# Kernel optimization log

Hardware: AMD Instinct MI355X
Metric: run time of the kernel (lower is better)

Reference implementation:

```python
import jax, jax.numpy as jnp
import numpy as np

N_HEAD = 16
LN_EPS = 1e-5


def _layernorm(x, g, b):
    mu = jnp.mean(x, axis=-1, keepdims=True)
    var = jnp.mean(jnp.square(x - mu), axis=-1, keepdims=True)
    return (x - mu) * jax.lax.rsqrt(var + LN_EPS) * g + b


def setup_inputs() -> dict:
    key = jax.random.key(0)
    ks = jax.random.split(key, 12)
    B, S, D = 2, 2048, 1024
    F = 4 * D
    std = 0.02
    return {
        "x": jax.random.normal(ks[0], (B, S, D), jnp.float32),
        "w_attn": jax.random.normal(ks[1], (D, 3 * D), jnp.float32) * std,
        "b_attn": jnp.zeros((3 * D,), jnp.float32),
        "w_o": jax.random.normal(ks[2], (D, D), jnp.float32) * std,
        "b_o": jnp.zeros((D,), jnp.float32),
        "ln1_g": jnp.ones((D,), jnp.float32),
        "ln1_b": jnp.zeros((D,), jnp.float32),
        "w_fc": jax.random.normal(ks[3], (D, F), jnp.float32) * std,
        "b_fc": jnp.zeros((F,), jnp.float32),
        "w_pr": jax.random.normal(ks[4], (F, D), jnp.float32) * std,
        "b_pr": jnp.zeros((D,), jnp.float32),
        "ln2_g": jnp.ones((D,), jnp.float32),
        "ln2_b": jnp.zeros((D,), jnp.float32),
    }


def reference(x, w_attn, b_attn, w_o, b_o, ln1_g, ln1_b,
              w_fc, b_fc, w_pr, b_pr, ln2_g, ln2_b):
    B, S, D = x.shape
    H = N_HEAD
    hd = D // H

    # --- attention ---
    qkv = x @ w_attn + b_attn                      # [B,S,3D]
    q, k, v = jnp.split(qkv, 3, axis=-1)
    q = q.reshape(B, S, H, hd).transpose(0, 2, 1, 3)  # [B,H,S,hd]
    k = k.reshape(B, S, H, hd).transpose(0, 2, 1, 3)
    v = v.reshape(B, S, H, hd).transpose(0, 2, 1, 3)

    # scores in fp32, scaled by sqrt(head_dim) (scale=True)
    w = jnp.einsum('bhqd,bhkd->bhqk', q.astype(jnp.float32),
                   k.astype(jnp.float32)) / jnp.sqrt(jnp.float32(hd))
    bias = jnp.tril(jnp.ones((S, S), jnp.float32))     # causal mask slice of registered buffer
    w = w * bias + (-10000.0) * (1.0 - bias)
    a = jax.nn.softmax(w, axis=-1).astype(v.dtype)
    o = jnp.einsum('bhqk,bhkd->bhqd', a, v)            # [B,H,S,hd]
    o = o.transpose(0, 2, 1, 3).reshape(B, S, D)
    a_out = o @ w_o + b_o

    # --- post-LN residual + MLP (gelu, d_ff = 4D) ---
    n = _layernorm(x + a_out, ln1_g, ln1_b)
    m = jax.nn.gelu(n @ w_fc + b_fc, approximate=False) @ w_pr + b_pr
    h = _layernorm(n + m, ln2_g, ln2_b)
    return h
```

## Files before the change

kernel.cpp:

```cpp
#include <hip/hip_runtime.h>
#include <stdint.h>
#include <math.h>


typedef __attribute__((ext_vector_type(4))) float f32x4;
typedef __attribute__((ext_vector_type(8))) short s16x8;

__device__ __forceinline__ float bf2f(short s){
  unsigned u = ((unsigned)(unsigned short)s) << 16;
  return __builtin_bit_cast(float, u);
}
__device__ __forceinline__ short f2bf(float f){
  unsigned u = __builtin_bit_cast(unsigned, f);
  unsigned r = (u + 0x7fffu + ((u >> 16) & 1u)) >> 16;
  return (short)(unsigned short)r;
}

__device__ __forceinline__ void gload_lds16(const void* gp, void* lp){
  __builtin_amdgcn_global_load_lds(
      (__attribute__((address_space(1))) void*)const_cast<void*>(gp),
      (__attribute__((address_space(3))) void*)lp,
      16, 0, 0);
}

__global__ void cvt_f32_bf16(const float* __restrict__ in, short* __restrict__ out, int n){
  int i = (blockIdx.x * blockDim.x + threadIdx.x) * 4;
  if (i < n){
    float4 v = *(const float4*)(in + i);
    short4 o;
    o.x = f2bf(v.x); o.y = f2bf(v.y); o.z = f2bf(v.z); o.w = f2bf(v.w);
    *(short4*)(out + i) = o;
  }
}

__global__ __launch_bounds__(256) void wtrans(const float* __restrict__ in,
                                              short* __restrict__ out, int R, int C){
  __shared__ float tile[32][33];
  int c0 = blockIdx.x * 32, r0 = blockIdx.y * 32;
  int tx = threadIdx.x, ty = threadIdx.y;
  #pragma unroll
  for (int j = 0; j < 4; ++j)
    tile[ty + j*8][tx] = in[(size_t)(r0 + ty + j*8) * C + c0 + tx];
  __syncthreads();
  #pragma unroll
  for (int j = 0; j < 4; ++j)
    out[(size_t)(c0 + ty + j*8) * R + r0 + tx] = f2bf(tile[tx][ty + j*8]);
}

__global__ __launch_bounds__(256) void vtrans(const short* __restrict__ qkv,
                                              short* __restrict__ vt){
  __shared__ short tile[32][33];
  int bh = blockIdx.z; int b = bh >> 4, h = bh & 15;
  int s0 = blockIdx.x * 32, d0 = blockIdx.y * 32;
  int tx = threadIdx.x, ty = threadIdx.y;
  #pragma unroll
  for (int j = 0; j < 4; ++j)
    tile[ty + j*8][tx] = qkv[(size_t)(b*2048 + s0 + ty + j*8) * 3072 + 2048 + h*64 + d0 + tx];
  __syncthreads();
  #pragma unroll
  for (int j = 0; j < 4; ++j)
    vt[(size_t)(bh*64 + d0 + ty + j*8) * 2048 + s0 + tx] = tile[tx][ty + j*8];
}

#define GBM 128
#define GBN 128
#define GBK 64

__global__ __launch_bounds__(256, 4) void gemm_bf16(
    const short* __restrict__ A, const short* __restrict__ BT,
    const float* __restrict__ bias,
    void* __restrict__ out, void* __restrict__ out2,
    void* __restrict__ out3, void* __restrict__ out4,
    int M, int N, int K, int EPI, int KS)
{
  __shared__ short sA[GBM * GBK];
  __shared__ short sB[GBN * GBK];
  const int t = threadIdx.x;
  const int lane = t & 63;
  const int w = t >> 6;
  const int wr = w >> 1, wc = w & 1;
  const int lrow = lane & 15;
  const int lk = lane >> 4;

  const int gx = gridDim.x;
  const int nwg = gx * gridDim.y;
  const int P = blockIdx.y * gx + blockIdx.x;
  const int wg = (P & 7) * (nwg >> 3) + (P >> 3);
  const int m0 = (wg / gx) * GBM, n0 = (wg % gx) * GBN;

  const int Kspl = K / KS;
  const int kbeg = blockIdx.z * Kspl;

  f32x4 acc[4][4] = {};

  for (int kk = kbeg; kk < kbeg + Kspl; kk += GBK){
    __syncthreads();
    #pragma unroll
    for (int r = 0; r < 4; ++r){
      int o = r * 4096 + t * 16;
      int row = o >> 7;
      int phys = (o >> 4) & 7;
      int lsl = phys ^ (row & 7);
      gload_lds16(A + (size_t)(m0 + row) * K + kk + lsl * 8, (char*)sA + o);
    }
    #pragma unroll
    for (int r = 0; r < 4; ++r){
      int o = r * 4096 + t * 16;
      int row = o >> 7;
      int phys = (o >> 4) & 7;
      int lsl = phys ^ (row & 7);
      gload_lds16(BT + (size_t)(n0 + row) * K + kk + lsl * 8, (char*)sB + o);
    }
    __syncthreads();

    #pragma unroll
    for (int kc = 0; kc < 2; ++kc){
      s16x8 af[4], bf[4];
      #pragma unroll
      for (int rt = 0; rt < 4; ++rt){
        int row = wr*64 + rt*16 + lrow;
        int slot = (kc*4 + lk) ^ (row & 7);
        af[rt] = *(const s16x8*)&sA[row*64 + slot*8];
      }
      #pragma unroll
      for (int ct = 0; ct < 4; ++ct){
        int row = wc*64 + ct*16 + lrow;
        int slot = (kc*4 + lk) ^ (row & 7);
        bf[ct] = *(const s16x8*)&sB[row*64 + slot*8];
      }
      #pragma unroll
      for (int rt = 0; rt < 4; ++rt)
        #pragma unroll
        for (int ct = 0; ct < 4; ++ct)
          acc[rt][ct] = __builtin_amdgcn_mfma_f32_16x16x32_bf16(af[rt], bf[ct], acc[rt][ct], 0, 0, 0);
    }
  }

  void* pz = (blockIdx.z == 0) ? out : (blockIdx.z == 1) ? out2
           : (blockIdx.z == 2) ? out3 : out4;
  #pragma unroll
  for (int rt = 0; rt < 4; ++rt){
    #pragma unroll
    for (int ct = 0; ct < 4; ++ct){
      #pragma unroll
      for (int r = 0; r < 4; ++r){
        int row = m0 + wr*64 + rt*16 + lk*4 + r;
        int col = n0 + wc*64 + ct*16 + lrow;
        size_t idx = (size_t)row * N + col;
        if (EPI == 4){
          ((short*)pz)[idx] = f2bf(acc[rt][ct][r]);
        } else {
          float v = acc[rt][ct][r] + bias[col];
          if (EPI == 0){
            ((short*)out)[idx] = f2bf(v);
          } else {
            float g = 0.5f * v * (1.0f + erff(v * 0.70710678118654752f));
            ((short*)out)[idx] = f2bf(g);
          }
        }
      }
    }
  }
}

__global__ __launch_bounds__(256, 2) void attn_kernel(
    const short* __restrict__ qkv, const short* __restrict__ vt,
    short* __restrict__ ob)
{
  const int P = blockIdx.x;
  const int xcd = P & 7;
  const int idx = P >> 3;
  const int pairi = idx & 15;
  const int bh = xcd + ((idx >> 4) << 3);
  const int b = bh >> 4, h = bh & 15;
  const int t  = threadIdx.x;
  const int lane = t & 63;
  const int w = t >> 6;
  const int lrow = lane & 15, lk = lane >> 4;

  __shared__ short sK[2][64*64];
  __shared__ short sV[2][64*64];
  __shared__ short sP[4][16][68];

  const size_t kgbase = (size_t)(b*2048)*3072 + 1024 + h*64;
  const size_t vgbase = (size_t)((b*16 + h)*64)*2048;

  s16x8 bones;
  #pragma unroll
  for (int i = 0; i < 8; ++i) bones[i] = (short)0x3F80;

  auto stage = [&](int buf, int k0){
    #pragma unroll
    for (int r2 = 0; r2 < 2; ++r2){
      int o = r2*4096 + t*16;
      int row = o >> 7;
      int lsl = ((o >> 4) & 7) ^ (row & 7);
      gload_lds16(qkv + kgbase + (size_t)(k0 + row)*3072 + lsl*8, (char*)sK[buf] + o);
      gload_lds16(vt  + vgbase + (size_t)row*2048 + k0   + lsl*8, (char*)sV[buf] + o);
    }
  };

  for (int pass = 0; pass < 2; ++pass){
    const int qt = pass ? 31 - pairi : pairi;
    const int q0 = qt * 64;
    const int qbase = q0 + w * 16;

    s16x8 aq[2];
    #pragma unroll
    for (int kc = 0; kc < 2; ++kc)
      aq[kc] = *(const s16x8*)(qkv + (size_t)(b*2048 + qbase + lrow)*3072 + h*64 + kc*32 + lk*8);

    f32x4 oacc[4] = {};
    f32x4 sumacc = {};

    const int nt = qt + 1;
    __syncthreads();
    stage(0, 0);
    __syncthreads();
    int cur = 0;

    for (int ktile = 0; ktile < nt; ++ktile){
      const int k0 = ktile * 64;
      if (ktile + 1 < nt) stage(cur ^ 1, k0 + 64);

      f32x4 sacc[4] = {};
      __builtin_amdgcn_s_setprio(1);
      #pragma unroll
      for (int kc = 0; kc < 2; ++kc){
        #pragma unroll
        for (int ct = 0; ct < 4; ++ct){
          int row = ct*16 + lrow;
          int slot = (kc*4 + lk) ^ (row & 7);
          s16x8 bk = *(const s16x8*)&sK[cur][row*64 + slot*8];
          sacc[ct] = __builtin_amdgcn_mfma_f32_16x16x32_bf16(aq[kc], bk, sacc[ct], 0, 0, 0);
        }
      }
      __builtin_amdgcn_s_setprio(0);

      const bool need_mask = (k0 + 63 > qbase);
      #pragma unroll
      for (int ct = 0; ct < 4; ++ct){
        #pragma unroll
        for (int r = 0; r < 4; ++r){
          float v = sacc[ct][r] * 0.125f;
          if (need_mask){
            int qi = qbase + lk*4 + r;
            int ki = k0 + ct*16 + lrow;
            if (ki > qi) v = -10000.0f;
          }
          sP[w][lk*4 + r][ct*16 + lrow] = f2bf(__expf(v));
        }
      }

      s16x8 pa[2];
      #pragma unroll
      for (int kc = 0; kc < 2; ++kc)
        pa[kc] = *(const s16x8*)&sP[w][lrow][kc*32 + lk*8];
      __builtin_amdgcn_s_setprio(1);
      #pragma unroll
      for (int dt = 0; dt < 4; ++dt){
        #pragma unroll
        for (int kc = 0; kc < 2; ++kc){
          int row = dt*16 + lrow;
          int slot = (kc*4 + lk) ^ (row & 7);
          s16x8 bv = *(const s16x8*)&sV[cur][row*64 + slot*8];
          oacc[dt] = __builtin_amdgcn_mfma_f32_16x16x32_bf16(pa[kc], bv, oacc[dt], 0, 0, 0);
        }
      }
      #pragma unroll
      for (int kc = 0; kc < 2; ++kc)
        sumacc = __builtin_amdgcn_mfma_f32_16x16x32_bf16(pa[kc], bones, sumacc, 0, 0, 0);
      __builtin_amdgcn_s_setprio(0);

      __syncthreads();
      cur ^= 1;
    }

    #pragma unroll
    for (int r = 0; r < 4; ++r){
      float inv = 1.0f / sumacc[r];
      int row = b*2048 + qbase + lk*4 + r;
      #pragma unroll
      for (int dt = 0; dt < 4; ++dt){
        int col = h*64 + dt*16 + lrow;
        ob[(size_t)row * 1024 + col] = f2bf(oacc[dt][r] * inv);
      }
    }
  }
}

__global__ __launch_bounds__(256) void ln_fused(
    const short* __restrict__ p0, const short* __restrict__ p1,
    const short* __restrict__ p2, const short* __restrict__ p3,
    const float* __restrict__ bias,
    const short* __restrict__ resid_bf, const float* __restrict__ resid_f,
    const float* __restrict__ g, const float* __restrict__ b,
    void* __restrict__ out, int bf16_out)
{
  const int row = blockIdx.x;
  const int t = threadIdx.x;
  const size_t base = (size_t)row*1024 + t*4;
  short4 a0 = *(const short4*)(p0 + base);
  short4 a1 = *(const short4*)(p1 + base);
  short4 a2 = *(const short4*)(p2 + base);
  short4 a3 = *(const short4*)(p3 + base);
  float4 bi = *(const float4*)(bias + t*4);
  float r0, r1, r2, r3;
  if (resid_bf){
    short4 rr = *(const short4*)(resid_bf + base);
    r0 = bf2f(rr.x); r1 = bf2f(rr.y); r2 = bf2f(rr.z); r3 = bf2f(rr.w);
  } else {
    float4 rr = *(const float4*)(resid_f + base);
    r0 = rr.x; r1 = rr.y; r2 = rr.z; r3 = rr.w;
  }
  float v0 = bf2f(a0.x) + bf2f(a1.x) + bf2f(a2.x) + bf2f(a3.x) + bi.x + r0;
  float v1 = bf2f(a0.y) + bf2f(a1.y) + bf2f(a2.y) + bf2f(a3.y) + bi.y + r1;
  float v2 = bf2f(a0.z) + bf2f(a1.z) + bf2f(a2.z) + bf2f(a3.z) + bi.z + r2;
  float v3 = bf2f(a0.w) + bf2f(a1.w) + bf2f(a2.w) + bf2f(a3.w) + bi.w + r3;
  float s = v0 + v1 + v2 + v3;
  float q = v0*v0 + v1*v1 + v2*v2 + v3*v3;
  #pragma unroll
  for (int off = 1; off < 64; off <<= 1){
    s += __shfl_xor(s, off, 64);
    q += __shfl_xor(q, off, 64);
  }
  __shared__ float ss[4], sq[4];
  if ((t & 63) == 0){ ss[t >> 6] = s; sq[t >> 6] = q; }
  __syncthreads();
  s = ss[0] + ss[1] + ss[2] + ss[3];
  q = sq[0] + sq[1] + sq[2] + sq[3];
  float mu = s * (1.0f/1024.0f);
  float var = q * (1.0f/1024.0f) - mu*mu;
  float rs = rsqrtf(var + 1e-5f);
  float4 gg = *(const float4*)(g + t*4);
  float4 bb = *(const float4*)(b + t*4);
  float o0 = (v0 - mu)*rs*gg.x + bb.x;
  float o1 = (v1 - mu)*rs*gg.y + bb.y;
  float o2 = (v2 - mu)*rs*gg.z + bb.z;
  float o3 = (v3 - mu)*rs*gg.w + bb.w;
  if (bf16_out){
    short4 o; o.x = f2bf(o0); o.y = f2bf(o1); o.z = f2bf(o2); o.w = f2bf(o3);
    *(short4*)((short*)out + base) = o;
  } else {
    float4 o = {o0, o1, o2, o3};
    *(float4*)((float*)out + base) = o;
  }
}

extern "C" void kernel_launch(void* const* d_in, const int* in_sizes, int n_in,
                              void* d_out, int out_size, void* d_ws, size_t ws_size,
                              hipStream_t stream) {
  const float* x      = (const float*)d_in[0];
  const float* w_attn = (const float*)d_in[1];
  const float* b_attn = (const float*)d_in[2];
  const float* w_o    = (const float*)d_in[3];
  const float* b_o    = (const float*)d_in[4];
  const float* ln1_g  = (const float*)d_in[5];
  const float* ln1_b  = (const float*)d_in[6];
  const float* w_fc   = (const float*)d_in[7];
  const float* b_fc   = (const float*)d_in[8];
  const float* w_pr   = (const float*)d_in[9];
  const float* b_pr   = (const float*)d_in[10];
  const float* ln2_g  = (const float*)d_in[11];
  const float* ln2_b  = (const float*)d_in[12];

  char* ws = (char*)d_ws;
  const size_t MB = 1048576;
  short* waT  = (short*)(ws + 0);
  short* wfT  = (short*)(ws + 6*MB);
  short* wpT  = (short*)(ws + 14*MB);
  short* woT  = (short*)(ws + 22*MB);
  short* xb   = (short*)(ws + 24*MB);
  short* vt   = (short*)(ws + 24*MB);
  short* pp2  = (short*)(ws + 24*MB);
  short* qkvb = (short*)(ws + 32*MB);
  short* fb   = (short*)(ws + 32*MB);
  short* ob   = (short*)(ws + 56*MB);
  short* pp0  = (short*)(ws + 64*MB);
  short* pp1  = (short*)(ws + 72*MB);
  short* nb   = (short*)(ws + 80*MB);
  short* pp3  = (short*)(ws + 88*MB);

  const int M = 4096;

  cvt_f32_bf16<<<dim3(M*1024/1024), dim3(256), 0, stream>>>(x, xb, M*1024);
  wtrans<<<dim3(3072/32, 1024/32), dim3(32,8), 0, stream>>>(w_attn, waT, 1024, 3072);
  wtrans<<<dim3(1024/32, 1024/32), dim3(32,8), 0, stream>>>(w_o,   woT, 1024, 1024);
  wtrans<<<dim3(4096/32, 1024/32), dim3(32,8), 0, stream>>>(w_fc,  wfT, 1024, 4096);
  wtrans<<<dim3(1024/32, 4096/32), dim3(32,8), 0, stream>>>(w_pr,  wpT, 4096, 1024);
  gemm_bf16<<<dim3(3072/GBN, M/GBM), dim3(256), 0, stream>>>(
      xb, waT, b_attn, qkvb, nullptr, nullptr, nullptr, M, 3072, 1024, 0, 1);
  vtrans<<<dim3(2048/32, 64/32, 32), dim3(32,8), 0, stream>>>(qkvb, vt);
  attn_kernel<<<dim3(512), dim3(256), 0, stream>>>(qkvb, vt, ob);
  gemm_bf16<<<dim3(1024/GBN, M/GBM, 4), dim3(256), 0, stream>>>(
      ob, woT, nullptr, pp0, pp1, pp2, pp3, M, 1024, 1024, 4, 4);
  ln_fused<<<dim3(M), dim3(256), 0, stream>>>(pp0, pp1, pp2, pp3, b_o,
                                              nullptr, x, ln1_g, ln1_b, nb, 1);
  gemm_bf16<<<dim3(4096/GBN, M/GBM), dim3(256), 0, stream>>>(
      nb, wfT, b_fc, fb, nullptr, nullptr, nullptr, M, 4096, 1024, 2, 1);
  gemm_bf16<<<dim3(1024/GBN, M/GBM, 4), dim3(256), 0, stream>>>(
      fb, wpT, nullptr, pp0, pp1, pp2, pp3, M, 1024, 4096, 4, 4);
  ln_fused<<<dim3(M), dim3(256), 0, stream>>>(pp0, pp1, pp2, pp3, b_pr,
                                              nb, nullptr, ln2_g, ln2_b, d_out, 0);
}
```

Before: 254.8 us.

## Stage GEMM epilogue through LDS, fold softmax scale into QKV, widen attention blocks

The GEMM epilogue now writes results into swizzled shared memory and then issues 16-byte coalesced global stores instead of scattered 2-byte stores. The QKV GEMM pre-multiplies Q by log2(e)/sqrt(hd), so attention can use exp2f without a per-score scale. The attention kernel now runs 512 threads: two warp sets process the paired short and long query tiles together over shared K/V stages. It also uses explicit vmcnt waits and raw barriers, so the next tile's loads overlap compute. These changes add shared-memory traffic and an extra barrier in the GEMM, and make the attention synchronisation more delicate.

```diff
diff --git a/kernel.cpp b/kernel.cpp
--- a/kernel.cpp
+++ b/kernel.cpp
@@ -22,6 +22,8 @@
       (__attribute__((address_space(3))) void*)lp,
       16, 0, 0);
 }
+
+#define QSCALE 0.18033688f
 
 __global__ void cvt_f32_bf16(const float* __restrict__ in, short* __restrict__ out, int n){
   int i = (blockIdx.x * blockDim.x + threadIdx.x) * 4;
@@ -73,8 +75,9 @@
     void* __restrict__ out3, void* __restrict__ out4,
     int M, int N, int K, int EPI, int KS)
 {
-  __shared__ short sA[GBM * GBK];
-  __shared__ short sB[GBN * GBK];
+  __shared__ __attribute__((aligned(16))) short smem[GBM*GBK*2];
+  short* sA = smem;
+  short* sB = smem + GBM*GBK;
   const int t = threadIdx.x;
   const int lane = t & 63;
   const int w = t >> 6;
@@ -136,42 +139,55 @@
     }
   }
 
-  void* pz = (blockIdx.z == 0) ? out : (blockIdx.z == 1) ? out2
-           : (blockIdx.z == 2) ? out3 : out4;
+  __syncthreads();
   #pragma unroll
   for (int rt = 0; rt < 4; ++rt){
     #pragma unroll
     for (int ct = 0; ct < 4; ++ct){
       #pragma unroll
       for (int r = 0; r < 4; ++r){
-        int row = m0 + wr*64 + rt*16 + lk*4 + r;
-        int col = n0 + wc*64 + ct*16 + lrow;
-        size_t idx = (size_t)row * N + col;
-        if (EPI == 4){
-          ((short*)pz)[idx] = f2bf(acc[rt][ct][r]);
-        } else {
-          float v = acc[rt][ct][r] + bias[col];
+        int row = wr*64 + rt*16 + lk*4 + r;
+        int col = wc*64 + ct*16 + lrow;
+        float v = acc[rt][ct][r];
+        if (EPI != 4){
+          v += bias[n0 + col];
           if (EPI == 0){
-            ((short*)out)[idx] = f2bf(v);
+            if (n0 + col < 1024) v *= QSCALE;
           } else {
-            float g = 0.5f * v * (1.0f + erff(v * 0.70710678118654752f));
-            ((short*)out)[idx] = f2bf(g);
+            v = 0.5f * v * (1.0f + erff(v * 0.70710678118654752f));
           }
         }
-      }
-    }
-  }
-}
-
-__global__ __launch_bounds__(256, 2) void attn_kernel(
+        int off = row*256 + ((col*2) ^ (((row >> 2) & 7) << 5));
+        *(short*)((char*)smem + off) = f2bf(v);
+      }
+    }
+  }
+  __syncthreads();
+  void* pz = (blockIdx.z == 0) ? out : (blockIdx.z == 1) ? out2
+           : (blockIdx.z == 2) ? out3 : out4;
+  short* outp = (EPI == 4) ? (short*)pz : (short*)out;
+  #pragma unroll
+  for (int j = 0; j < 8; ++j){
+    int L = j*4096 + t*16;
+    int row = L >> 8;
+    int cb  = L & 255;
+    int phys = row*256 + (cb ^ (((row >> 2) & 7) << 5));
+    s16x8 vv = *(const s16x8*)((char*)smem + phys);
+    *(s16x8*)(outp + (size_t)(m0 + row) * N + n0 + (cb >> 1)) = vv;
+  }
+}
+
+__global__ __launch_bounds__(512, 4) void attn_kernel(
     const short* __restrict__ qkv, const short* __restrict__ vt,
     short* __restrict__ ob)
 {
   const int P = blockIdx.x;
   const int xcd = P & 7;
   const int idx = P >> 3;
-  const int pairi = idx & 15;
-  const int bh = xcd + ((idx >> 4) << 3);
+  const int raw = idx & 15;
+  const int grp = idx >> 4;
+  const int pairi = (grp & 2) ? (15 - raw) : raw;
+  const int bh = xcd + (grp << 3);
   const int b = bh >> 4, h = bh & 15;
   const int t  = threadIdx.x;
   const int lane = t & 63;
@@ -180,7 +196,7 @@
 
   __shared__ short sK[2][64*64];
   __shared__ short sV[2][64*64];
-  __shared__ short sP[4][16][68];
+  __shared__ short sP[8][16][68];
 
   const size_t kgbase = (size_t)(b*2048)*3072 + 1024 + h*64;
   const size_t vgbase = (size_t)((b*16 + h)*64)*2048;
@@ -190,39 +206,42 @@
   for (int i = 0; i < 8; ++i) bones[i] = (short)0x3F80;
 
   auto stage = [&](int buf, int k0){
-    #pragma unroll
-    for (int r2 = 0; r2 < 2; ++r2){
-      int o = r2*4096 + t*16;
-      int row = o >> 7;
-      int lsl = ((o >> 4) & 7) ^ (row & 7);
-      gload_lds16(qkv + kgbase + (size_t)(k0 + row)*3072 + lsl*8, (char*)sK[buf] + o);
-      gload_lds16(vt  + vgbase + (size_t)row*2048 + k0   + lsl*8, (char*)sV[buf] + o);
-    }
+    int o = t*16;
+    int row = o >> 7;
+    int lsl = ((o >> 4) & 7) ^ (row & 7);
+    gload_lds16(qkv + kgbase + (size_t)(k0 + row)*3072 + lsl*8, (char*)sK[buf] + o);
+    gload_lds16(vt  + vgbase + (size_t)row*2048 + k0   + lsl*8, (char*)sV[buf] + o);
   };
 
-  for (int pass = 0; pass < 2; ++pass){
-    const int qt = pass ? 31 - pairi : pairi;
-    const int q0 = qt * 64;
-    const int qbase = q0 + w * 16;
-
-    s16x8 aq[2];
-    #pragma unroll
-    for (int kc = 0; kc < 2; ++kc)
-      aq[kc] = *(const s16x8*)(qkv + (size_t)(b*2048 + qbase + lrow)*3072 + h*64 + kc*32 + lk*8);
-
-    f32x4 oacc[4] = {};
-    f32x4 sumacc = {};
-
-    const int nt = qt + 1;
-    __syncthreads();
-    stage(0, 0);
-    __syncthreads();
-    int cur = 0;
-
-    for (int ktile = 0; ktile < nt; ++ktile){
-      const int k0 = ktile * 64;
-      if (ktile + 1 < nt) stage(cur ^ 1, k0 + 64);
-
+  const int set = w >> 2;
+  const int qt = set ? (31 - pairi) : pairi;
+  const int qbase = qt*64 + (w & 3)*16;
+  const int ntSelf = qt + 1;
+  const int ntB = 32 - pairi;
+
+  s16x8 aq[2];
+  #pragma unroll
+  for (int kc = 0; kc < 2; ++kc)
+    aq[kc] = *(const s16x8*)(qkv + (size_t)(b*2048 + qbase + lrow)*3072 + h*64 + kc*32 + lk*8);
+
+  f32x4 oacc[4] = {};
+  f32x4 sumacc = {};
+
+  stage(0, 0);
+  int cur = 0;
+
+  for (int ktile = 0; ktile < ntB; ++ktile){
+    const int k0 = ktile * 64;
+    if (ktile + 1 < ntB){
+      stage(cur ^ 1, k0 + 64);
+      asm volatile("s_waitcnt vmcnt(2)" ::: "memory");
+    } else {
+      asm volatile("s_waitcnt vmcnt(0)" ::: "memory");
+    }
+    __builtin_amdgcn_s_barrier();
+    __builtin_amdgcn_sched_barrier(0);
+
+    if (ktile < ntSelf){
       f32x4 sacc[4] = {};
       __builtin_amdgcn_s_setprio(1);
       #pragma unroll
@@ -242,13 +261,13 @@
       for (int ct = 0; ct < 4; ++ct){
         #pragma unroll
         for (int r = 0; r < 4; ++r){
-          float v = sacc[ct][r] * 0.125f;
+          float v = sacc[ct][r];
           if (need_mask){
             int qi = qbase + lk*4 + r;
             int ki = k0 + ct*16 + lrow;
-            if (ki > qi) v = -10000.0f;
+            if (ki > qi) v = -100000.0f;
           }
-          sP[w][lk*4 + r][ct*16 + lrow] = f2bf(__expf(v));
+          sP[w][lk*4 + r][ct*16 + lrow] = f2bf(exp2f(v));
         }
       }
 
@@ -271,20 +290,21 @@
       for (int kc = 0; kc < 2; ++kc)
         sumacc = __builtin_amdgcn_mfma_f32_16x16x32_bf16(pa[kc], bones, sumacc, 0, 0, 0);
       __builtin_amdgcn_s_setprio(0);
-
-      __syncthreads();
-      cur ^= 1;
-    }
-
+    }
+
+    __builtin_amdgcn_sched_barrier(0);
+    __builtin_amdgcn_s_barrier();
+    cur ^= 1;
+  }
+
+  #pragma unroll
+  for (int r = 0; r < 4; ++r){
+    float inv = 1.0f / sumacc[r];
+    int row = b*2048 + qbase + lk*4 + r;
     #pragma unroll
-    for (int r = 0; r < 4; ++r){
-      float inv = 1.0f / sumacc[r];
-      int row = b*2048 + qbase + lk*4 + r;
-      #pragma unroll
-      for (int dt = 0; dt < 4; ++dt){
-        int col = h*64 + dt*16 + lrow;
-        ob[(size_t)row * 1024 + col] = f2bf(oacc[dt][r] * inv);
-      }
+    for (int dt = 0; dt < 4; ++dt){
+      int col = h*64 + dt*16 + lrow;
+      ob[(size_t)row * 1024 + col] = f2bf(oacc[dt][r] * inv);
     }
   }
 }
@@ -391,7 +411,7 @@
   gemm_bf16<<<dim3(3072/GBN, M/GBM), dim3(256), 0, stream>>>(
       xb, waT, b_attn, qkvb, nullptr, nullptr, nullptr, M, 3072, 1024, 0, 1);
   vtrans<<<dim3(2048/32, 64/32, 32), dim3(32,8), 0, stream>>>(qkvb, vt);
-  attn_kernel<<<dim3(512), dim3(256), 0, stream>>>(qkvb, vt, ob);
+  attn_kernel<<<dim3(512), dim3(512), 0, stream>>>(qkvb, vt, ob);
   gemm_bf16<<<dim3(1024/GBN, M/GBM, 4), dim3(256), 0, stream>>>(
       ob, woT, nullptr, pp0, pp1, pp2, pp3, M, 1024, 1024, 4, 4);
   ln_fused<<<dim3(M), dim3(256), 0, stream>>>(pp0, pp1, pp2, pp3, b_o,
```

Result: no change. 256.3 us (+0.6%).
